# Kernel optimization log

Hardware: AMD Instinct MI355X
Metric: run time of the kernel (lower is better)

## Reference

```python
import jax, jax.numpy as jnp
import numpy as np

B, NF, D = 8192, 64, 128


def setup_inputs() -> dict:
    key = jax.random.key(0)
    k1, k2, k3, k4 = jax.random.split(key, 4)
    F = jax.random.normal(k1, (B, NF, D), dtype=jnp.float32)
    # interaction weight tensor (num_fields, num_fields, embedding_dim)
    W = jax.random.normal(k2, (NF, NF, D), dtype=jnp.float32) * 0.05
    # torch Linear weights (out_features, in_features); y = x @ W.T
    K_w = jax.random.normal(k3, (D, D), dtype=jnp.float32) * (1.0 / np.sqrt(D))
    Q_w = jax.random.normal(k4, (D, D), dtype=jnp.float32) * (1.0 / np.sqrt(D))
    return {"F": F, "W": W, "K_w": K_w, "Q_w": Q_w}


def reference(F, W, K_w, Q_w):
    # K(F): torch Linear without bias -> F @ K_w.T, shape [B, NF, D]
    Kf = jnp.einsum('bjd,ed->bje', F, K_w)
    # S = bmm(F, K(F)^T) -> [B, NF, NF]
    S = jnp.einsum('bid,bjd->bij', F, Kf)
    # (S.unsqueeze(-1) * W).sum(dim=2) without materializing [B,NF,NF,D]
    out = jnp.einsum('bij,ijd->bid', S, W)
    # residual: Q(F)
    out = out + jnp.einsum('bid,ed->bie', F, Q_w)
    return out
```

## Files before the change

kernel.cpp:

```cpp
#include <hip/hip_runtime.h>
#include <stdint.h>

typedef _Float16 f16x8 __attribute__((ext_vector_type(8)));
typedef _Float16 f16x4 __attribute__((ext_vector_type(4)));
typedef float    f32x4 __attribute__((ext_vector_type(4)));

#define NFIELD 64
#define DIM    128
#define BTOT   8192

__global__ void prep_kernel(const float* __restrict__ W,
                            const float* __restrict__ Kw,
                            const float* __restrict__ Qw,
                            _Float16* __restrict__ Wt,
                            _Float16* __restrict__ Kh,
                            _Float16* __restrict__ Qh) {
  const int blk = blockIdx.x, t = threadIdx.x;
  if (blk < NFIELD) {
    const float* Wi = W + (size_t)blk * NFIELD * DIM;
    _Float16* Wo = Wt + (size_t)blk * DIM * NFIELD;
    for (int idx = t; idx < DIM * NFIELD; idx += 256) {
      int d = idx >> 6, j = idx & 63;
      Wo[idx] = (_Float16)Wi[j * DIM + d];
    }
  } else if (blk == NFIELD) {
    for (int idx = t; idx < DIM * DIM; idx += 256) Kh[idx] = (_Float16)Kw[idx];
  } else {
    for (int idx = t; idx < DIM * DIM; idx += 256) Qh[idx] = (_Float16)Qw[idx];
  }
}

__global__ __launch_bounds__(256, 3)
void s_kernel(const float* __restrict__ F,
              const _Float16* __restrict__ Kh,
              _Float16* __restrict__ Sg, int c0) {
  __shared__ _Float16 sF[64 * 136];
  __shared__ float    sKf[64 * 132];
  const int t = threadIdx.x;
  const int lane = t & 63, wave = t >> 6;
  const int l15 = lane & 15, quad = lane >> 4;
  const int b = c0 + blockIdx.x;
  const float* Fb = F + (size_t)b * (NFIELD * DIM);

  for (int idx = t; idx < 2048; idx += 256) {
    float4 v = ((const float4*)Fb)[idx];
    int row = idx >> 5, c4 = idx & 31;
    f16x4 h;
    h[0] = (_Float16)v.x; h[1] = (_Float16)v.y; h[2] = (_Float16)v.z; h[3] = (_Float16)v.w;
    *(f16x4*)&sF[row * 136 + c4 * 4] = h;
  }
  __syncthreads();

  f16x8 afK[4];
#pragma unroll
  for (int kt = 0; kt < 4; ++kt)
    afK[kt] = *(const f16x8*)&sF[(wave * 16 + l15) * 136 + kt * 32 + quad * 8];
#pragma unroll
  for (int et = 0; et < 8; ++et) {
    const _Float16* kp = Kh + (et * 16 + l15) * DIM + quad * 8;
    f32x4 acc = {0.f, 0.f, 0.f, 0.f};
#pragma unroll
    for (int kt = 0; kt < 4; ++kt) {
      f16x8 bf = *(const f16x8*)(kp + kt * 32);
      acc = __builtin_amdgcn_mfma_f32_16x16x32_f16(afK[kt], bf, acc, 0, 0, 0);
    }
    float* op = &sKf[(wave * 16 + quad * 4) * 132 + et * 16 + l15];
    op[0] = acc[0]; op[132] = acc[1]; op[264] = acc[2]; op[396] = acc[3];
  }
  __syncthreads();

  f32x4 accS[4];
#pragma unroll
  for (int it = 0; it < 4; ++it) accS[it] = (f32x4){0.f, 0.f, 0.f, 0.f};
#pragma unroll
  for (int kt = 0; kt < 4; ++kt) {
    const float* bp = &sKf[(wave * 16 + l15) * 132 + kt * 32 + quad * 8];
    float4 b0 = *(const float4*)bp;
    float4 b1 = *(const float4*)(bp + 4);
    f16x8 bf;
    bf[0] = (_Float16)b0.x; bf[1] = (_Float16)b0.y; bf[2] = (_Float16)b0.z; bf[3] = (_Float16)b0.w;
    bf[4] = (_Float16)b1.x; bf[5] = (_Float16)b1.y; bf[6] = (_Float16)b1.z; bf[7] = (_Float16)b1.w;
#pragma unroll
    for (int it = 0; it < 4; ++it) {
      f16x8 af = *(const f16x8*)&sF[(it * 16 + l15) * 136 + kt * 32 + quad * 8];
      accS[it] = __builtin_amdgcn_mfma_f32_16x16x32_f16(af, bf, accS[it], 0, 0, 0);
    }
  }
  _Float16* Sb = Sg + (size_t)blockIdx.x * (NFIELD * NFIELD);
#pragma unroll
  for (int it = 0; it < 4; ++it)
#pragma unroll
    for (int r = 0; r < 4; ++r)
      Sb[(it * 16 + quad * 4 + r) * 64 + wave * 16 + l15] = (_Float16)accS[it][r];
}

__global__ __launch_bounds__(256, 3)
void out_kernel(const float* __restrict__ F,
                const _Float16* __restrict__ Sg,
                const _Float16* __restrict__ Wt,
                const _Float16* __restrict__ Qh,
                float* __restrict__ Out, int c0) {
  __shared__ _Float16 sBt[128 * 200];
  const int i = blockIdx.y;
  const int t = threadIdx.x;
  const int lane = t & 63, wave = t >> 6;
  const int l15 = lane & 15, quad = lane >> 4;

  const f16x8* wp = (const f16x8*)(Wt + (size_t)i * DIM * NFIELD);
  for (int idx = t; idx < 1024; idx += 256) {
    int d = idx >> 3, jw = idx & 7;
    *(f16x8*)&sBt[d * 200 + jw * 8] = wp[idx];
  }
  const f16x8* qp = (const f16x8*)Qh;
  for (int idx = t; idx < 2048; idx += 256) {
    int d = idx >> 4, ew = idx & 15;
    *(f16x8*)&sBt[d * 200 + 64 + ew * 8] = qp[idx];
  }
  __syncthreads();

  f32x4 acc[2][8];
#pragma unroll
  for (int mi = 0; mi < 2; ++mi)
#pragma unroll
    for (int nt = 0; nt < 8; ++nt) acc[mi][nt] = (f32x4){0.f, 0.f, 0.f, 0.f};

  const int bl0 = blockIdx.x * 128;
#pragma unroll
  for (int kt = 0; kt < 6; ++kt) {
    f16x8 af[2];
#pragma unroll
    for (int mi = 0; mi < 2; ++mi) {
      const int bl = bl0 + (wave * 2 + mi) * 16 + l15;
      if (kt < 2) {
        const int j0 = kt * 32 + quad * 8;
        af[mi] = *(const f16x8*)(Sg + (size_t)bl * 4096 + i * 64 + j0);
      } else {
        const int e0 = (kt - 2) * 32 + quad * 8;
        const float* fp = F + ((size_t)(c0 + bl) * NFIELD + i) * DIM + e0;
        float4 f0 = *(const float4*)fp;
        float4 f1 = *(const float4*)(fp + 4);
        f16x8 a;
        a[0] = (_Float16)f0.x; a[1] = (_Float16)f0.y; a[2] = (_Float16)f0.z; a[3] = (_Float16)f0.w;
        a[4] = (_Float16)f1.x; a[5] = (_Float16)f1.y; a[6] = (_Float16)f1.z; a[7] = (_Float16)f1.w;
        af[mi] = a;
      }
    }
#pragma unroll
    for (int nt = 0; nt < 8; ++nt) {
      f16x8 bf = *(const f16x8*)&sBt[(nt * 16 + l15) * 200 + kt * 32 + quad * 8];
      acc[0][nt] = __builtin_amdgcn_mfma_f32_16x16x32_f16(af[0], bf, acc[0][nt], 0, 0, 0);
      acc[1][nt] = __builtin_amdgcn_mfma_f32_16x16x32_f16(af[1], bf, acc[1][nt], 0, 0, 0);
    }
  }

#pragma unroll
  for (int mi = 0; mi < 2; ++mi) {
    const int blr = bl0 + (wave * 2 + mi) * 16 + quad * 4;
#pragma unroll
    for (int nt = 0; nt < 8; ++nt) {
      const int d = nt * 16 + l15;
#pragma unroll
      for (int r = 0; r < 4; ++r) {
        const size_t gb = (size_t)(c0 + blr + r);
        Out[(gb * NFIELD + i) * DIM + d] = acc[mi][nt][r];
      }
    }
  }
}

extern "C" void kernel_launch(void* const* d_in, const int* in_sizes, int n_in,
                              void* d_out, int out_size, void* d_ws, size_t ws_size,
                              hipStream_t stream) {
  const float* F  = (const float*)d_in[0];
  const float* W  = (const float*)d_in[1];
  const float* Kw = (const float*)d_in[2];
  const float* Qw = (const float*)d_in[3];
  float* Out = (float*)d_out;

  _Float16* Wt = (_Float16*)d_ws;
  _Float16* Kh = Wt + (size_t)NFIELD * DIM * NFIELD;
  _Float16* Qh = Kh + DIM * DIM;
  _Float16* Sg = Qh + DIM * DIM;
  const size_t fixed_bytes = ((size_t)NFIELD * DIM * NFIELD + 2 * DIM * DIM) * sizeof(_Float16);
  size_t avail = (ws_size > fixed_bytes) ? (ws_size - fixed_bytes) : 0;
  int CB = BTOT;
  while (CB > 128 && (size_t)CB * NFIELD * NFIELD * sizeof(_Float16) > avail) CB >>= 1;

  prep_kernel<<<dim3(NFIELD + 2), 256, 0, stream>>>(W, Kw, Qw, Wt, Kh, Qh);
  for (int c0 = 0; c0 < BTOT; c0 += CB) {
    s_kernel<<<dim3(CB), 256, 0, stream>>>(F, Kh, Sg, c0);
    out_kernel<<<dim3(CB / 128, NFIELD), 256, 0, stream>>>(F, Sg, Wt, Qh, Out, c0);
  }
}
```

Before: 653.6 us.

## Split S computation into separate Kf GEMM and per-wave S kernels

The fused per-batch S kernel, which staged F and Kf in shared memory, is replaced by two kernels. The first is a flat GEMM computing Kf = F·Kᵀ in fp16 into a workspace buffer. The second computes S with one wave per batch element, reading F and Kf straight from global memory with no LDS and no block barriers. This removes the shared-memory round trips and syncs and raises occupancy, at the cost of writing and reading an extra Kf intermediate, reading F an extra time, and needing more workspace per chunk.

```diff
diff --git a/kernel.cpp b/kernel.cpp
--- a/kernel.cpp
+++ b/kernel.cpp
@@ -30,68 +30,99 @@
   }
 }
 
-__global__ __launch_bounds__(256, 3)
-void s_kernel(const float* __restrict__ F,
-              const _Float16* __restrict__ Kh,
-              _Float16* __restrict__ Sg, int c0) {
-  __shared__ _Float16 sF[64 * 136];
-  __shared__ float    sKf[64 * 132];
+__global__ __launch_bounds__(256, 4)
+void kf_kernel(const float* __restrict__ F,
+               const _Float16* __restrict__ Kh,
+               _Float16* __restrict__ Kf, int c0) {
   const int t = threadIdx.x;
   const int lane = t & 63, wave = t >> 6;
   const int l15 = lane & 15, quad = lane >> 4;
-  const int b = c0 + blockIdx.x;
-  const float* Fb = F + (size_t)b * (NFIELD * DIM);
-
-  for (int idx = t; idx < 2048; idx += 256) {
-    float4 v = ((const float4*)Fb)[idx];
-    int row = idx >> 5, c4 = idx & 31;
-    f16x4 h;
-    h[0] = (_Float16)v.x; h[1] = (_Float16)v.y; h[2] = (_Float16)v.z; h[3] = (_Float16)v.w;
-    *(f16x4*)&sF[row * 136 + c4 * 4] = h;
-  }
-  __syncthreads();
-
-  f16x8 afK[4];
-#pragma unroll
-  for (int kt = 0; kt < 4; ++kt)
-    afK[kt] = *(const f16x8*)&sF[(wave * 16 + l15) * 136 + kt * 32 + quad * 8];
-#pragma unroll
-  for (int et = 0; et < 8; ++et) {
-    const _Float16* kp = Kh + (et * 16 + l15) * DIM + quad * 8;
-    f32x4 acc = {0.f, 0.f, 0.f, 0.f};
-#pragma unroll
-    for (int kt = 0; kt < 4; ++kt) {
-      f16x8 bf = *(const f16x8*)(kp + kt * 32);
-      acc = __builtin_amdgcn_mfma_f32_16x16x32_f16(afK[kt], bf, acc, 0, 0, 0);
-    }
-    float* op = &sKf[(wave * 16 + quad * 4) * 132 + et * 16 + l15];
-    op[0] = acc[0]; op[132] = acc[1]; op[264] = acc[2]; op[396] = acc[3];
-  }
-  __syncthreads();
-
-  f32x4 accS[4];
-#pragma unroll
-  for (int it = 0; it < 4; ++it) accS[it] = (f32x4){0.f, 0.f, 0.f, 0.f};
+  const int m0 = blockIdx.x * 128 + wave * 32;
+
+  f32x4 acc[2][8];
+#pragma unroll
+  for (int mi = 0; mi < 2; ++mi)
+#pragma unroll
+    for (int nt = 0; nt < 8; ++nt) acc[mi][nt] = (f32x4){0.f, 0.f, 0.f, 0.f};
+
+  const size_t gm0 = (size_t)c0 * NFIELD + m0;
 #pragma unroll
   for (int kt = 0; kt < 4; ++kt) {
-    const float* bp = &sKf[(wave * 16 + l15) * 132 + kt * 32 + quad * 8];
-    float4 b0 = *(const float4*)bp;
-    float4 b1 = *(const float4*)(bp + 4);
-    f16x8 bf;
-    bf[0] = (_Float16)b0.x; bf[1] = (_Float16)b0.y; bf[2] = (_Float16)b0.z; bf[3] = (_Float16)b0.w;
-    bf[4] = (_Float16)b1.x; bf[5] = (_Float16)b1.y; bf[6] = (_Float16)b1.z; bf[7] = (_Float16)b1.w;
+    f16x8 af[2];
+#pragma unroll
+    for (int mi = 0; mi < 2; ++mi) {
+      const float* fp = F + (gm0 + mi * 16 + l15) * DIM + kt * 32 + quad * 8;
+      float4 f0 = *(const float4*)fp;
+      float4 f1 = *(const float4*)(fp + 4);
+      f16x8 a;
+      a[0] = (_Float16)f0.x; a[1] = (_Float16)f0.y; a[2] = (_Float16)f0.z; a[3] = (_Float16)f0.w;
+      a[4] = (_Float16)f1.x; a[5] = (_Float16)f1.y; a[6] = (_Float16)f1.z; a[7] = (_Float16)f1.w;
+      af[mi] = a;
+    }
+#pragma unroll
+    for (int nt = 0; nt < 8; ++nt) {
+      f16x8 bf = *(const f16x8*)(Kh + (nt * 16 + l15) * DIM + kt * 32 + quad * 8);
+      acc[0][nt] = __builtin_amdgcn_mfma_f32_16x16x32_f16(af[0], bf, acc[0][nt], 0, 0, 0);
+      acc[1][nt] = __builtin_amdgcn_mfma_f32_16x16x32_f16(af[1], bf, acc[1][nt], 0, 0, 0);
+    }
+  }
+#pragma unroll
+  for (int mi = 0; mi < 2; ++mi)
+#pragma unroll
+    for (int nt = 0; nt < 8; ++nt)
+#pragma unroll
+      for (int r = 0; r < 4; ++r)
+        Kf[(size_t)(m0 + mi * 16 + quad * 4 + r) * DIM + nt * 16 + l15] =
+            (_Float16)acc[mi][nt][r];
+}
+
+__global__ __launch_bounds__(256, 4)
+void s2_kernel(const float* __restrict__ F,
+               const _Float16* __restrict__ Kf,
+               _Float16* __restrict__ Sg, int c0) {
+  const int t = threadIdx.x;
+  const int lane = t & 63, wave = t >> 6;
+  const int l15 = lane & 15, quad = lane >> 4;
+  const int bl = blockIdx.x * 4 + wave;
+  const float* Fb = F + ((size_t)(c0 + bl) * NFIELD) * DIM;
+  const _Float16* Kb = Kf + (size_t)bl * NFIELD * DIM;
+
+  f32x4 acc[4][4];
+#pragma unroll
+  for (int it = 0; it < 4; ++it)
+#pragma unroll
+    for (int jt = 0; jt < 4; ++jt) acc[it][jt] = (f32x4){0.f, 0.f, 0.f, 0.f};
+
+#pragma unroll
+  for (int kt = 0; kt < 4; ++kt) {
+    const int k0 = kt * 32 + quad * 8;
+    f16x8 af[4], bf[4];
 #pragma unroll
     for (int it = 0; it < 4; ++it) {
-      f16x8 af = *(const f16x8*)&sF[(it * 16 + l15) * 136 + kt * 32 + quad * 8];
-      accS[it] = __builtin_amdgcn_mfma_f32_16x16x32_f16(af, bf, accS[it], 0, 0, 0);
-    }
-  }
-  _Float16* Sb = Sg + (size_t)blockIdx.x * (NFIELD * NFIELD);
+      const float* fp = Fb + (it * 16 + l15) * DIM + k0;
+      float4 f0 = *(const float4*)fp;
+      float4 f1 = *(const float4*)(fp + 4);
+      f16x8 a;
+      a[0] = (_Float16)f0.x; a[1] = (_Float16)f0.y; a[2] = (_Float16)f0.z; a[3] = (_Float16)f0.w;
+      a[4] = (_Float16)f1.x; a[5] = (_Float16)f1.y; a[6] = (_Float16)f1.z; a[7] = (_Float16)f1.w;
+      af[it] = a;
+      bf[it] = *(const f16x8*)(Kb + (it * 16 + l15) * DIM + k0);
+    }
+#pragma unroll
+    for (int it = 0; it < 4; ++it)
+#pragma unroll
+      for (int jt = 0; jt < 4; ++jt)
+        acc[it][jt] = __builtin_amdgcn_mfma_f32_16x16x32_f16(af[it], bf[jt], acc[it][jt], 0, 0, 0);
+  }
+
+  _Float16* Sb = Sg + (size_t)bl * (NFIELD * NFIELD);
 #pragma unroll
   for (int it = 0; it < 4; ++it)
 #pragma unroll
-    for (int r = 0; r < 4; ++r)
-      Sb[(it * 16 + quad * 4 + r) * 64 + wave * 16 + l15] = (_Float16)accS[it][r];
+    for (int jt = 0; jt < 4; ++jt)
+#pragma unroll
+      for (int r = 0; r < 4; ++r)
+        Sb[(it * 16 + quad * 4 + r) * 64 + jt * 16 + l15] = (_Float16)acc[it][jt][r];
 }
 
 __global__ __launch_bounds__(256, 3)
@@ -180,15 +211,18 @@
   _Float16* Wt = (_Float16*)d_ws;
   _Float16* Kh = Wt + (size_t)NFIELD * DIM * NFIELD;
   _Float16* Qh = Kh + DIM * DIM;
-  _Float16* Sg = Qh + DIM * DIM;
+  _Float16* Kf = Qh + DIM * DIM;
   const size_t fixed_bytes = ((size_t)NFIELD * DIM * NFIELD + 2 * DIM * DIM) * sizeof(_Float16);
+  const size_t per_batch = ((size_t)NFIELD * DIM + NFIELD * NFIELD) * sizeof(_Float16);
   size_t avail = (ws_size > fixed_bytes) ? (ws_size - fixed_bytes) : 0;
   int CB = BTOT;
-  while (CB > 128 && (size_t)CB * NFIELD * NFIELD * sizeof(_Float16) > avail) CB >>= 1;
+  while (CB > 128 && (size_t)CB * per_batch > avail) CB >>= 1;
+  _Float16* Sg = Kf + (size_t)CB * NFIELD * DIM;
 
   prep_kernel<<<dim3(NFIELD + 2), 256, 0, stream>>>(W, Kw, Qw, Wt, Kh, Qh);
   for (int c0 = 0; c0 < BTOT; c0 += CB) {
-    s_kernel<<<dim3(CB), 256, 0, stream>>>(F, Kh, Sg, c0);
+    kf_kernel<<<dim3(CB / 2), 256, 0, stream>>>(F, Kh, Kf, c0);
+    s2_kernel<<<dim3(CB / 4), 256, 0, stream>>>(F, Kf, Sg, c0);
     out_kernel<<<dim3(CB / 128, NFIELD), 256, 0, stream>>>(F, Sg, Wt, Qh, Out, c0);
   }
 }
```

Measured after the change: 704.3 us. +7.7%, slower.
